# Performance work log

Hardware: AMD Instinct MI355X
Metric: run time of the kernel (lower is better)

## Reference

```python
import math
import jax, jax.numpy as jnp
import numpy as np

B, H, W = 2, 128, 128
HW = H * W
D, NH, NL, KS = 256, 8, 1, 5
NP = KS * KS
HD = D // NH
DFF = 1024
KEEP = 0.25
H_SIZE = 188.0
EPS = 1e-5


def _layernorm(x, g, b):
    m = x.mean(-1, keepdims=True)
    v = ((x - m) ** 2).mean(-1, keepdims=True)
    return (x - m) * jax.lax.rsqrt(v + EPS) * g + b


def _mha(q_in, k_in, v_in, w_qkv, b_qkv, w_o, b_o):
    wq, wk, wv = jnp.split(w_qkv, 3, axis=0)
    bq, bk, bv = jnp.split(b_qkv, 3, axis=0)
    def heads(x, w, b):
        y = x @ w.T + b
        return y.reshape(y.shape[0], y.shape[1], NH, HD)
    q, k, v = heads(q_in, wq, bq), heads(k_in, wk, bk), heads(v_in, wv, bv)
    scores = jnp.einsum('bqhd,bkhd->bhqk', q, k) / math.sqrt(HD)
    attn = jax.nn.softmax(scores, axis=-1)
    out = jnp.einsum('bhqk,bkhd->bqhd', attn, v).reshape(q_in.shape[0], q_in.shape[1], D)
    return out @ w_o.T + b_o


def _bilinear(v, grid):
    # v: (B, HW, NH, HD); grid: (B, LQ, NH, NP, 2) normalized (x, y) in [0,1]
    x = grid[..., 0] * W - 0.5
    y = grid[..., 1] * H - 0.5
    x0 = jnp.floor(x); y0 = jnp.floor(y)
    lx = x - x0; ly = y - y0
    x0i = x0.astype(jnp.int32); y0i = y0.astype(jnp.int32)
    bidx = jnp.arange(v.shape[0])[:, None, None, None]
    hidx = jnp.arange(NH)[None, None, :, None]
    def corner(xi, yi, wgt):
        valid = (xi >= 0) & (xi < W) & (yi >= 0) & (yi < H)  # zero-pad outside
        idx = jnp.clip(yi, 0, H - 1) * W + jnp.clip(xi, 0, W - 1)
        s = v[bidx, idx, hidx]  # (B, LQ, NH, NP, HD)
        return s * (wgt * valid)[..., None]
    return (corner(x0i, y0i, (1 - lx) * (1 - ly))
            + corner(x0i + 1, y0i, lx * (1 - ly))
            + corner(x0i, y0i + 1, (1 - lx) * ly)
            + corner(x0i + 1, y0i + 1, lx * ly))


def _where_to_attend(query, ref_windows, lbw, lbb, sow, sob, kernel_indices):
    Bq, L = ref_windows.shape[:2]
    ob = (query @ lbw.T + lbb).reshape(Bq, L, NH, NL, 4)  # with_rotation=False -> 4 vars
    rw = ref_windows[:, :, None, None, :]  # (B, L, 1, 1, 7)
    ref_boxes = rw[..., jnp.array([0, 1, 3, 4])]
    ref_angles = rw[..., 6:7]
    angles = jnp.broadcast_to(ref_angles, (Bq, L, NH, NL, 1))
    boxes = ref_boxes + ob / 8.0 * ref_boxes[..., jnp.array([2, 3, 2, 3])]
    center = boxes[..., None, :2]  # (B, L, NH, NL, 1, 2)
    size = boxes[..., None, 2:]
    cos_a, sin_a = jnp.cos(angles), jnp.sin(angles)
    rot = jnp.stack([cos_a, -sin_a, sin_a, cos_a], -1).reshape(Bq, L, NH, NL, 1, 2, 2)
    dgrid = (query @ sow.T + sob).reshape(Bq, L, NH, NL, NP, 2) / H_SIZE
    fg = kernel_indices * jax.nn.relu(size)              # (B, L, NH, NL, NP, 2)
    fg = center + (fg[..., None, :] * rot).sum(-1)       # rotate then shift
    return fg + dgrid


def _box_attn(query, value, ref_windows, vpw, vpb, law, lab, lbw, lbb, sow, sob, ow, ob_, kernel_indices):
    Bq, LQ = query.shape[:2]
    LV = value.shape[1]
    v = (value @ vpw.T + vpb).reshape(Bq, LV, NH, HD)
    aw = jax.nn.softmax((query @ law.T + lab).reshape(Bq, LQ, NH, NL * NP), axis=-1)
    aw = aw.reshape(Bq, LQ, NH, NL, NP)
    grid = _where_to_attend(query, ref_windows, lbw, lbb, sow, sob, kernel_indices)
    sampled = _bilinear(v, grid[:, :, :, 0])             # single level (NL=1)
    out = (aw[:, :, :, 0, :, None] * sampled).sum(-2).reshape(Bq, LQ, D)
    return out @ ow.T + ob_


def _forward(src, pos, ref_windows, score_mask, in_proj_w, in_proj_b, mha_out_w, mha_out_b,
             value_proj_w, value_proj_b, linear_attn_w, linear_attn_b, linear_box_w, linear_box_b,
             samp_off_w, samp_off_b, ca_out_w, ca_out_b, lin1_w, lin1_b, lin2_w, lin2_b,
             qn_g, qn_b, n1_g, n1_b, n2_g, n2_b, kernel_indices):
    Bq = src.shape[0]
    fg_num = math.ceil(src.shape[1] * KEEP)
    sel_score, indices = jax.lax.top_k(score_mask, fg_num)
    gather = lambda x, i: jnp.take_along_axis(x, i[..., None], axis=1)
    sel_src = gather(src, indices)
    sel_pos = gather(pos, indices)
    sel_ref = gather(ref_windows, indices)
    q_num = math.ceil(fg_num * KEEP)
    q_idx = jax.lax.top_k(sel_score, q_num)[1]
    q_src = gather(sel_src, q_idx)
    q_pos = gather(sel_pos, q_idx)
    qk = q_src + q_pos
    q2 = _mha(qk, qk, q_src, in_proj_w, in_proj_b, mha_out_w, mha_out_b)
    q_src = _layernorm(q_src + q2, qn_g, qn_b)
    brow = jnp.arange(Bq)[:, None]
    sel_src = sel_src.at[brow, q_idx].set(q_src)
    src2 = _box_attn(sel_src + sel_pos, src, sel_ref, value_proj_w, value_proj_b,
                     linear_attn_w, linear_attn_b, linear_box_w, linear_box_b,
                     samp_off_w, samp_off_b, ca_out_w, ca_out_b, kernel_indices)
    sel_src = _layernorm(sel_src + src2, n1_g, n1_b)
    ff = jax.nn.relu(sel_src @ lin1_w.T + lin1_b) @ lin2_w.T + lin2_b
    sel_src = _layernorm(sel_src + ff, n2_g, n2_b)
    return src.at[brow, indices].set(sel_src)


def setup_inputs() -> dict:
    key = jax.random.key(0)
    ks = jax.random.split(key, 16)
    def w(k, shape):
        return jax.random.normal(k, shape, dtype=jnp.float32) * 0.02
    # deformable sampling-offsets bias init (per-head directional grid)
    thetas = np.arange(NH) * (2.0 * np.pi / NH)
    g = np.stack([np.cos(thetas), np.sin(thetas)], -1)
    g = g / np.abs(g).max(-1, keepdims=True)
    g = np.tile(g.reshape(NH, 1, 1, 2), (1, NL, NP, 1)) * (np.arange(NP) + 1).reshape(1, 1, NP, 1)
    samp_off_b = jnp.asarray(g.reshape(-1), dtype=jnp.float32)
    # fixed kernel indices buffer (odd kernel, (x,y) order, /kernel_size)
    ind = np.linspace(-(KS - 1) / 2, (KS - 1) / 2, KS)
    ii, jj = np.meshgrid(ind, ind, indexing='ij')
    kernel_indices = jnp.asarray(np.stack([jj, ii], -1).reshape(-1, 2) / KS, dtype=jnp.float32)
    return dict(
        src=jax.random.normal(ks[0], (B, HW, D), dtype=jnp.float32),
        pos=jax.random.normal(ks[1], (B, HW, D), dtype=jnp.float32),
        src_shape=jnp.array([[H, W]], dtype=jnp.int32),
        src_start_idx=jnp.zeros((1,), dtype=jnp.int32),
        ref_windows=jax.random.uniform(ks[2], (B, HW, 7), dtype=jnp.float32),
        score_mask=jax.random.normal(ks[3], (B, HW), dtype=jnp.float32),
        in_proj_w=w(ks[4], (3 * D, D)), in_proj_b=jnp.zeros((3 * D,), jnp.float32),
        mha_out_w=w(ks[5], (D, D)), mha_out_b=jnp.zeros((D,), jnp.float32),
        value_proj_w=w(ks[6], (D, D)), value_proj_b=jnp.zeros((D,), jnp.float32),
        linear_attn_w=w(ks[7], (NH * NL * NP, D)), linear_attn_b=jnp.zeros((NH * NL * NP,), jnp.float32),
        linear_box_w=w(ks[8], (NL * NH * 4, D)), linear_box_b=jnp.zeros((NL * NH * 4,), jnp.float32),
        samp_off_w=w(ks[9], (NH * NL * NP * 2, D)), samp_off_b=samp_off_b,
        ca_out_w=w(ks[10], (D, D)), ca_out_b=jnp.zeros((D,), jnp.float32),
        lin1_w=w(ks[11], (DFF, D)), lin1_b=jnp.zeros((DFF,), jnp.float32),
        lin2_w=w(ks[12], (D, DFF)), lin2_b=jnp.zeros((D,), jnp.float32),
        qn_g=jnp.ones((D,), jnp.float32), qn_b=jnp.zeros((D,), jnp.float32),
        n1_g=jnp.ones((D,), jnp.float32), n1_b=jnp.zeros((D,), jnp.float32),
        n2_g=jnp.ones((D,), jnp.float32), n2_b=jnp.zeros((D,), jnp.float32),
        kernel_indices=kernel_indices,
    )


def reference(src, pos, src_shape, src_start_idx, ref_windows, score_mask,
              in_proj_w, in_proj_b, mha_out_w, mha_out_b, value_proj_w, value_proj_b,
              linear_attn_w, linear_attn_b, linear_box_w, linear_box_b, samp_off_w, samp_off_b,
              ca_out_w, ca_out_b, lin1_w, lin1_b, lin2_w, lin2_b,
              qn_g, qn_b, n1_g, n1_b, n2_g, n2_b, kernel_indices):
    # src_shape/src_start_idx are static single-level metadata (H, W closed over)
    return _forward(src, pos, ref_windows, score_mask, in_proj_w, in_proj_b, mha_out_w, mha_out_b,
                    value_proj_w, value_proj_b, linear_attn_w, linear_attn_b, linear_box_w, linear_box_b,
                    samp_off_w, samp_off_b, ca_out_w, ca_out_b, lin1_w, lin1_b, lin2_w, lin2_b,
                    qn_g, qn_b, n1_g, n1_b, n2_g, n2_b, kernel_indices)
```

## Files before the change

### kernel.cpp

```cpp
#include <hip/hip_runtime.h>
#include <hip/hip_bf16.h>
#include <math.h>

#define HW_N   16384
#define DIM    256
#define NSEL   4096
#define NQ     1024
#define NHEAD  8
#define HD     32
#define NP_    25
#define DFF_   1024

#define OFF_SELREF  8448LL
#define OFF_SELSRC  65792LL
#define OFF_SELPOS  2162944LL
#define OFF_QUERY   4260096LL
#define OFF_BIG     6357248LL
#define OFF_WBF     10551552LL
#define OFF_F       14745856LL

__device__ __forceinline__ unsigned int f2s(float f) {
    unsigned int u = __float_as_uint(f);
    return (u & 0x80000000u) ? ~u : (u | 0x80000000u);
}

typedef __bf16 bf16x8 __attribute__((ext_vector_type(8)));
typedef __bf16 bf16x4 __attribute__((ext_vector_type(4)));
typedef float  f32x4  __attribute__((ext_vector_type(4)));

extern "C" __global__ __launch_bounds__(256)
void wcvt_kernel(const float* __restrict__ s0, const float* __restrict__ s1,
                 const float* __restrict__ s2, const float* __restrict__ s3,
                 const float* __restrict__ s4, const float* __restrict__ s5,
                 const float* __restrict__ s6, const float* __restrict__ s7,
                 const float* __restrict__ s8, __hip_bfloat16* __restrict__ dst) {
    const long long g = (long long)blockIdx.x * 256 + threadIdx.x;
    const float* s; long long base;
    if      (g < 196608)  { s = s0; base = 0; }
    else if (g < 262144)  { s = s1; base = 196608; }
    else if (g < 327680)  { s = s2; base = 262144; }
    else if (g < 378880)  { s = s3; base = 327680; }
    else if (g < 387072)  { s = s4; base = 378880; }
    else if (g < 489472)  { s = s5; base = 387072; }
    else if (g < 555008)  { s = s6; base = 489472; }
    else if (g < 817152)  { s = s7; base = 555008; }
    else                  { s = s8; base = 817152; }
    dst[g] = __float2bfloat16(s[g - base]);
}

extern "C" __global__ __launch_bounds__(512)
void topk_hist_kernel(const float* __restrict__ score, unsigned int* __restrict__ hist) {
    const int t = threadIdx.x, bx = blockIdx.x, bb = blockIdx.y;
    const int i = bx * 512 + t;
    unsigned int u = f2s(score[(long long)bb * HW_N + i]);
    atomicAdd(&hist[bb * 8192 + (u >> 19)], 1u);
}

extern "C" __global__ __launch_bounds__(1024)
void topk_scan_kernel(const unsigned int* __restrict__ hist, unsigned int* __restrict__ ctrl) {
    __shared__ unsigned int scan[1024];
    const int t = threadIdx.x, bb = blockIdx.x;
    unsigned int loc[8]; unsigned int lsum = 0u;
    #pragma unroll
    for (int k = 0; k < 8; ++k) { loc[k] = hist[bb * 8192 + t * 8 + k]; lsum += loc[k]; }
    scan[t] = lsum;
    __syncthreads();
    for (int off = 1; off < 1024; off <<= 1) {
        unsigned int v = (t + off < 1024) ? scan[t + off] : 0u;
        __syncthreads();
        scan[t] += v;
        __syncthreads();
    }
    unsigned int nxt = (t < 1023) ? scan[t + 1] : 0u;
    unsigned int run = nxt;
    for (int k = 7; k >= 0; --k) {
        run += loc[k];
        unsigned int above = run - loc[k];
        if (run >= 1024u && above < 1024u) { ctrl[bb * 16 + 0] = (unsigned)(t * 8 + k); ctrl[bb * 16 + 1] = 1024u - above; }
        if (run >= 4096u && above < 4096u) { ctrl[bb * 16 + 2] = (unsigned)(t * 8 + k); ctrl[bb * 16 + 3] = 4096u - above; }
    }
}

extern "C" __global__ __launch_bounds__(1024)
void topk_collect_kernel(const float* __restrict__ score, unsigned int* __restrict__ ctrl,
                         unsigned long long* __restrict__ list1,
                         unsigned long long* __restrict__ list2) {
    const int t = threadIdx.x, bx = blockIdx.x, bb = blockIdx.y;
    const int i = bx * 1024 + t;
    const unsigned int T1 = ctrl[bb * 16 + 0], T2 = ctrl[bb * 16 + 2];
    unsigned int u = f2s(score[(long long)bb * HW_N + i]);
    unsigned int bin = u >> 19;
    unsigned long long key = ((unsigned long long)u << 32) | (unsigned int)(~(unsigned int)i);
    if (bin == T1) {
        unsigned int p = atomicAdd(&ctrl[bb * 16 + 4], 1u);
        if (p < 2048u) list1[bb * 2048 + p] = key;
    }
    if (bin == T2 && T2 != T1) {
        unsigned int p = atomicAdd(&ctrl[bb * 16 + 5], 1u);
        if (p < 2048u) list2[bb * 2048 + p] = key;
    }
}

extern "C" __global__ __launch_bounds__(1024)
void topk_classify_kernel(const float* __restrict__ score, unsigned int* __restrict__ ctrl,
                          const unsigned long long* __restrict__ list1,
                          const unsigned long long* __restrict__ list2,
                          int* __restrict__ idx_out) {
    __shared__ unsigned int cA, cB, baseA, baseB;
    const int t = threadIdx.x, bx = blockIdx.x, bb = blockIdx.y;
    const int i = bx * 1024 + t;
    if (t == 0) { cA = 0u; cB = 0u; }
    __syncthreads();
    const unsigned int T1 = ctrl[bb * 16 + 0], need1 = ctrl[bb * 16 + 1];
    const unsigned int T2 = ctrl[bb * 16 + 2], need2 = ctrl[bb * 16 + 3];
    const unsigned int c1 = min(ctrl[bb * 16 + 4], 2048u);
    const unsigned int c2 = min(ctrl[bb * 16 + 5], 2048u);
    unsigned int u = f2s(score[(long long)bb * HW_N + i]);
    unsigned int bin = u >> 19;
    unsigned long long key = ((unsigned long long)u << 32) | (unsigned int)(~(unsigned int)i);
    bool inA = false, inB = false;
    if (bin > T1) {
        inA = true;
    } else if (bin == T1) {
        unsigned int r = 0;
        for (unsigned int q = 0; q < c1; ++q) r += (list1[bb * 2048 + q] > key) ? 1u : 0u;
        if (r < need1) inA = true;
        else if (T2 == T1) inB = (r < need2);
        else inB = true;
    } else if (bin > T2) {
        inB = true;
    } else if (bin == T2) {
        unsigned int r = 0;
        for (unsigned int q = 0; q < c2; ++q) r += (list2[bb * 2048 + q] > key) ? 1u : 0u;
        inB = (r < need2);
    }
    unsigned int sA = 0u, sB = 0u;
    if (inA) sA = atomicAdd(&cA, 1u);
    if (inB) sB = atomicAdd(&cB, 1u);
    __syncthreads();
    if (t == 0) {
        baseA = atomicAdd(&ctrl[bb * 16 + 6], cA);
        baseB = atomicAdd(&ctrl[bb * 16 + 7], cB);
    }
    __syncthreads();
    if (inA) idx_out[bb * NSEL + baseA + sA] = i;
    if (inB) idx_out[bb * NSEL + 1024 + baseB + sB] = i;
}

extern "C" __global__ __launch_bounds__(256)
void gather_kernel(const float* __restrict__ src, const float* __restrict__ pos,
                   const float* __restrict__ refw, const int* __restrict__ idx,
                   float* __restrict__ selsrc, float* __restrict__ selpos,
                   float* __restrict__ selref, float* __restrict__ qk) {
    const int s = blockIdx.x, bb = blockIdx.y, t = threadIdx.x;
    const int i = idx[bb * NSEL + s];
    const long long so = ((long long)(bb * NSEL + s)) * DIM;
    const long long go = ((long long)(bb * HW_N + i)) * DIM;
    float sv = src[go + t], pv = pos[go + t];
    selsrc[so + t] = sv;
    selpos[so + t] = pv;
    if (s < NQ) qk[((long long)(bb * NQ + s)) * DIM + t] = sv + pv;
    if (t < 7)
        selref[(long long)(bb * NSEL + s) * 7 + t] = refw[(long long)(bb * HW_N + i) * 7 + t];
}

extern "C" __global__ __launch_bounds__(256)
void gemm_kernel(const void* __restrict__ Avp, long long sA,
                 const __hip_bfloat16* __restrict__ W, const float* __restrict__ bias,
                 float* __restrict__ C, long long sC,
                 int M, int N, int K, int relu, int omode, int amode) {
    __shared__ __hip_bfloat16 As[64][72];
    __shared__ __hip_bfloat16 Ws[64][72];
    const int t = threadIdx.x;
    const int n0 = blockIdx.x * 64, m0 = blockIdx.y * 64;
    const long long zoff = (long long)blockIdx.z * sC;
    const int lane = t & 63, wv = t >> 6;
    const int mw = (wv >> 1) * 32, nw = (wv & 1) * 32;
    const int fr = lane & 15;
    const int fk = (lane >> 4) * 8;
    const int sr = t >> 2;
    const int sk = (t & 3) * 16;

    f32x4 acc[2][2];
    #pragma unroll
    for (int i = 0; i < 2; ++i)
        #pragma unroll
        for (int j = 0; j < 2; ++j) acc[i][j] = {0.f, 0.f, 0.f, 0.f};

    const bool wok = (n0 + sr) < N;
    for (int k0 = 0; k0 < K; k0 += 64) {
        uint4 wa = make_uint4(0u, 0u, 0u, 0u), wb = make_uint4(0u, 0u, 0u, 0u);
        if (wok) {
            const __hip_bfloat16* wp = W + (long long)(n0 + sr) * K + k0 + sk;
            wa = *(const uint4*)wp;
            wb = *(const uint4*)(wp + 8);
        }
        if (amode) {
            const __hip_bfloat16* ap = (const __hip_bfloat16*)Avp
                + (long long)blockIdx.z * sA + (long long)(m0 + sr) * K + k0 + sk;
            uint4 aa = *(const uint4*)ap;
            uint4 ab = *(const uint4*)(ap + 8);
            __syncthreads();
            *(uint4*)&As[sr][sk] = aa;
            *(uint4*)&As[sr][sk + 8] = ab;
            *(uint4*)&Ws[sr][sk] = wa;
            *(uint4*)&Ws[sr][sk + 8] = wb;
        } else {
            const float* ap = (const float*)Avp
                + (long long)blockIdx.z * sA + (long long)(m0 + sr) * K + k0 + sk;
            float av[16];
            #pragma unroll
            for (int q = 0; q < 4; ++q) {
                float4 v = *(const float4*)(ap + q * 4);
                av[q * 4 + 0] = v.x; av[q * 4 + 1] = v.y; av[q * 4 + 2] = v.z; av[q * 4 + 3] = v.w;
            }
            __syncthreads();
            #pragma unroll
            for (int q = 0; q < 16; ++q) As[sr][sk + q] = __float2bfloat16(av[q]);
            *(uint4*)&Ws[sr][sk] = wa;
            *(uint4*)&Ws[sr][sk + 8] = wb;
        }
        __syncthreads();
        #pragma unroll
        for (int kk = 0; kk < 64; kk += 32) {
            bf16x8 a0 = *(const bf16x8*)&As[mw + fr][kk + fk];
            bf16x8 a1 = *(const bf16x8*)&As[mw + 16 + fr][kk + fk];
            bf16x8 b0 = *(const bf16x8*)&Ws[nw + fr][kk + fk];
            bf16x8 b1 = *(const bf16x8*)&Ws[nw + 16 + fr][kk + fk];
            acc[0][0] = __builtin_amdgcn_mfma_f32_16x16x32_bf16(a0, b0, acc[0][0], 0, 0, 0);
            acc[0][1] = __builtin_amdgcn_mfma_f32_16x16x32_bf16(a0, b1, acc[0][1], 0, 0, 0);
            acc[1][0] = __builtin_amdgcn_mfma_f32_16x16x32_bf16(a1, b0, acc[1][0], 0, 0, 0);
            acc[1][1] = __builtin_amdgcn_mfma_f32_16x16x32_bf16(a1, b1, acc[1][1], 0, 0, 0);
        }
    }
    const int crow = (lane >> 4) * 4;
    #pragma unroll
    for (int mi = 0; mi < 2; ++mi) {
        #pragma unroll
        for (int ni = 0; ni < 2; ++ni) {
            const int col = n0 + nw + ni * 16 + fr;
            if (col < N) {
                const float bv = bias ? bias[col] : 0.f;
                #pragma unroll
                for (int r = 0; r < 4; ++r) {
                    const int row = m0 + mw + mi * 16 + crow + r;
                    float v = acc[mi][ni][r] + bv;
                    if (relu) v = fmaxf(v, 0.f);
                    if (omode == 0) {
                        C[zoff + (long long)row * N + col] = v;
                    } else if (omode == 1) {
                        ((__hip_bfloat16*)C)[zoff + (long long)row * N + col] = __float2bfloat16(v);
                    } else if (omode == 2) {
                        ((__hip_bfloat16*)C)[zoff + (long long)col * M + row] = __float2bfloat16(v);
                    } else {
                        ((__hip_bfloat16*)C)[zoff + ((long long)(col >> 5) * 16384 + row) * 32 + (col & 31)]
                            = __float2bfloat16(v);
                    }
                }
            }
        }
    }
}

extern "C" __global__ __launch_bounds__(256)
void attn_kernel(const __hip_bfloat16* __restrict__ qkb,
                 const __hip_bfloat16* __restrict__ vT,
                 float* __restrict__ attout) {
    __shared__ __hip_bfloat16 pb[16][1048];
    __shared__ float redm[4][16];
    __shared__ float reds[4][16];
    __shared__ float redo[4][16][33];
    const int t = threadIdx.x;
    const int qt = blockIdx.x, h = blockIdx.y, bb = blockIdx.z;
    const int q0 = qt * 16;
    const int lane = t & 63, wv = t >> 6;
    const int fr = lane & 15, g = lane >> 4;
    const int kbase = wv * 256;
    const float scale = 0.17677669529663687f;

    bf16x8 qfrag = *(const bf16x8*)(qkb + ((long long)(bb * NQ + q0 + fr)) * 512 + h * HD + g * 8);

    f32x4 sfr[16];
    #pragma unroll
    for (int kt = 0; kt < 16; ++kt) {
        const int key0 = kbase + kt * 16;
        bf16x8 kf = *(const bf16x8*)(qkb + ((long long)(bb * NQ + key0 + fr)) * 512 + 256 + h * HD + g * 8);
        f32x4 z = {0.f, 0.f, 0.f, 0.f};
        sfr[kt] = __builtin_amdgcn_mfma_f32_16x16x32_bf16(qfrag, kf, z, 0, 0, 0);
    }
    #pragma unroll
    for (int kt = 0; kt < 16; ++kt)
        #pragma unroll
        for (int r = 0; r < 4; ++r) sfr[kt][r] *= scale;

    #pragma unroll
    for (int r = 0; r < 4; ++r) {
        float mx = -1e30f;
        #pragma unroll
        for (int kt = 0; kt < 16; ++kt) mx = fmaxf(mx, sfr[kt][r]);
        #pragma unroll
        for (int mm = 1; mm <= 8; mm <<= 1) mx = fmaxf(mx, __shfl_xor(mx, mm, 64));
        float sm = 0.f;
        #pragma unroll
        for (int kt = 0; kt < 16; ++kt) sm += expf(sfr[kt][r] - mx);
        #pragma unroll
        for (int mm = 1; mm <= 8; mm <<= 1) sm += __shfl_xor(sm, mm, 64);
        if (fr == 0) { redm[wv][4 * g + r] = mx; reds[wv][4 * g + r] = sm; }
    }
    __syncthreads();

    float gm[4], gl[4];
    #pragma unroll
    for (int r = 0; r < 4; ++r) {
        const int q = 4 * g + r;
        float mm = fmaxf(fmaxf(redm[0][q], redm[1][q]), fmaxf(redm[2][q], redm[3][q]));
        float ll = 0.f;
        #pragma unroll
        for (int w2 = 0; w2 < 4; ++w2) ll += reds[w2][q] * expf(redm[w2][q] - mm);
        gm[r] = mm; gl[r] = 1.f / ll;
    }
    #pragma unroll
    for (int kt = 0; kt < 16; ++kt) {
        #pragma unroll
        for (int r = 0; r < 4; ++r) {
            float p = expf(sfr[kt][r] - gm[r]) * gl[r];
            pb[4 * g + r][kbase + kt * 16 + fr] = __float2bfloat16(p);
        }
    }

    f32x4 o0 = {0.f, 0.f, 0.f, 0.f}, o1 = {0.f, 0.f, 0.f, 0.f};
    const __hip_bfloat16* vbase = vT + ((long long)bb * DIM + h * HD) * 1024;
    #pragma unroll
    for (int ks = 0; ks < 8; ++ks) {
        const int key0 = kbase + ks * 32 + g * 8;
        bf16x8 pf = *(const bf16x8*)&pb[fr][key0];
        bf16x8 v0 = *(const bf16x8*)(vbase + (long long)fr * 1024 + key0);
        bf16x8 v1 = *(const bf16x8*)(vbase + (long long)(16 + fr) * 1024 + key0);
        o0 = __builtin_amdgcn_mfma_f32_16x16x32_bf16(pf, v0, o0, 0, 0, 0);
        o1 = __builtin_amdgcn_mfma_f32_16x16x32_bf16(pf, v1, o1, 0, 0, 0);
    }

    #pragma unroll
    for (int r = 0; r < 4; ++r) {
        redo[wv][4 * g + r][fr] = o0[r];
        redo[wv][4 * g + r][16 + fr] = o1[r];
    }
    __syncthreads();
    #pragma unroll
    for (int i = 0; i < 2; ++i) {
        const int idx = t + i * 256;
        const int q = idx >> 5, d = idx & 31;
        float v = redo[0][q][d] + redo[1][q][d] + redo[2][q][d] + redo[3][q][d];
        attout[((long long)(bb * NQ + q0 + q)) * DIM + h * HD + d] = v;
    }
}

extern "C" __global__ __launch_bounds__(256)
void ln_kernel(const float* __restrict__ X, long long sx,
               const float* __restrict__ R, long long sr,
               const float* __restrict__ g, const float* __restrict__ bta,
               float* __restrict__ O, long long so) {
    __shared__ float red[4];
    const int row = blockIdx.x, bb = blockIdx.y, t = threadIdx.x;
    float x = X[(long long)bb * sx + (long long)row * DIM + t]
            + R[(long long)bb * sr + (long long)row * DIM + t];
    float v = x;
    #pragma unroll
    for (int m = 32; m >= 1; m >>= 1) v += __shfl_xor(v, m, 64);
    if ((t & 63) == 0) red[t >> 6] = v;
    __syncthreads();
    float mean = (red[0] + red[1] + red[2] + red[3]) * (1.f / 256.f);
    __syncthreads();
    float d = x - mean;
    v = d * d;
    #pragma unroll
    for (int m = 32; m >= 1; m >>= 1) v += __shfl_xor(v, m, 64);
    if ((t & 63) == 0) red[t >> 6] = v;
    __syncthreads();
    float var = (red[0] + red[1] + red[2] + red[3]) * (1.f / 256.f);
    O[(long long)bb * so + (long long)row * DIM + t] = d * rsqrtf(var + 1e-5f) * g[t] + bta[t];
}

extern "C" __global__ __launch_bounds__(256)
void addq_kernel(const float* __restrict__ a, const float* __restrict__ b2, float* __restrict__ o) {
    long long i = (long long)blockIdx.x * 256 + threadIdx.x;
    o[i] = a[i] + b2[i];
}

extern "C" __global__ __launch_bounds__(256)
void boxattn_kernel(const float* __restrict__ aw, const float* __restrict__ ob,
                    const float* __restrict__ dgrid, const float* __restrict__ selref,
                    const __hip_bfloat16* __restrict__ vp, const float* __restrict__ kidx,
                    float* __restrict__ boxout) {
    __shared__ float aw_s[200];
    __shared__ float ob_s[32];
    __shared__ float ref_s[7];
    __shared__ float ki_s[50];
    __shared__ float box_s[8][6];
    __shared__ float mx_s[8];
    __shared__ float inv_s[8];
    __shared__ float wq_s[200];
    __shared__ int   i4_s[800];
    __shared__ float w4_s[800];
    __shared__ float red4[4][8][32];
    const int t = threadIdx.x;
    const int s = blockIdx.x, bb = blockIdx.y;
    const long long base = (long long)(bb * NSEL + s);
    if (t < 200) aw_s[t] = aw[base * 200 + t];
    if (t < 32)  ob_s[t] = ob[base * 32 + t];
    if (t < 7)   ref_s[t] = selref[base * 7 + t];
    if (t < 50)  ki_s[t] = kidx[t];
    __syncthreads();

    if (t < 8) {
        float mx = -1e30f;
        #pragma unroll
        for (int p = 0; p < NP_; ++p) mx = fmaxf(mx, aw_s[t * NP_ + p]);
        mx_s[t] = mx;
        const float r0 = ref_s[0], r1 = ref_s[1], r3 = ref_s[3], r4 = ref_s[4], r6 = ref_s[6];
        box_s[t][0] = r0 + ob_s[t * 4 + 0] * 0.125f * r3;
        box_s[t][1] = r1 + ob_s[t * 4 + 1] * 0.125f * r4;
        box_s[t][2] = fmaxf(r3 + ob_s[t * 4 + 2] * 0.125f * r3, 0.f);
        box_s[t][3] = fmaxf(r4 + ob_s[t * 4 + 3] * 0.125f * r4, 0.f);
        box_s[t][4] = cosf(r6);
        box_s[t][5] = sinf(r6);
    }
    __syncthreads();

    if (t < 200) {
        const int h = t / NP_, p = t - h * NP_;
        const float w = expf(aw_s[t] - mx_s[h]);
        wq_s[t] = w;
        const float cx = box_s[h][0], cy = box_s[h][1];
        const float sw = box_s[h][2], sh = box_s[h][3];
        const float ca = box_s[h][4], sa = box_s[h][5];
        const float fx = ki_s[p * 2 + 0] * sw;
        const float fy = ki_s[p * 2 + 1] * sh;
        const float gx = cx + ca * fx - sa * fy + dgrid[base * 400 + 2 * t + 0] * (1.f / 188.f);
        const float gy = cy + sa * fx + ca * fy + dgrid[base * 400 + 2 * t + 1] * (1.f / 188.f);
        const float x = gx * 128.f - 0.5f;
        const float y = gy * 128.f - 0.5f;
        const float x0f = floorf(x), y0f = floorf(y);
        const float lx = x - x0f, ly = y - y0f;
        const int x0 = (int)x0f, y0 = (int)y0f;
        #pragma unroll
        for (int c = 0; c < 4; ++c) {
            const int xi = x0 + (c & 1);
            const int yi = y0 + (c >> 1);
            const float wgt = ((c & 1) ? lx : 1.f - lx) * ((c >> 1) ? ly : 1.f - ly);
            const bool valid = (xi >= 0) & (xi < 128) & (yi >= 0) & (yi < 128);
            const int cxi = min(max(xi, 0), 127);
            const int cyi = min(max(yi, 0), 127);
            i4_s[t * 4 + c] = cyi * 128 + cxi;
            w4_s[t * 4 + c] = w * (valid ? wgt : 0.f);
        }
    }
    __syncthreads();
    if (t < 8) {
        float sm = 0.f;
        #pragma unroll
        for (int p = 0; p < NP_; ++p) sm += wq_s[t * NP_ + p];
        inv_s[t] = 1.f / sm;
    }
    __syncthreads();

    {
        const int lane = t & 63, wv = t >> 6;
        const int h2 = lane >> 3, q = lane & 7;
        const __hip_bfloat16* vb = vp + ((long long)(bb * 8 + h2) * 16384) * 32 + q * 4;
        float a0 = 0.f, a1 = 0.f, a2 = 0.f, a3 = 0.f;
        for (int j = wv; j < 100; j += 4) {
            const int e = h2 * 100 + j;
            const int pix = i4_s[e];
            const float w = w4_s[e];
            bf16x4 v = *(const bf16x4*)(vb + (long long)pix * 32);
            a0 += w * (float)v[0];
            a1 += w * (float)v[1];
            a2 += w * (float)v[2];
            a3 += w * (float)v[3];
        }
        red4[wv][h2][q * 4 + 0] = a0;
        red4[wv][h2][q * 4 + 1] = a1;
        red4[wv][h2][q * 4 + 2] = a2;
        red4[wv][h2][q * 4 + 3] = a3;
    }
    __syncthreads();
    {
        const int h = t >> 5, d = t & 31;
        float v = red4[0][h][d] + red4[1][h][d] + red4[2][h][d] + red4[3][h][d];
        boxout[base * DIM + h * HD + d] = v * inv_s[h];
    }
}

extern "C" __global__ __launch_bounds__(256)
void scatter_kernel(const int* __restrict__ idx, const float* __restrict__ sel,
                    float* __restrict__ out) {
    const int s = blockIdx.x, bb = blockIdx.y, t = threadIdx.x;
    const int i = idx[bb * NSEL + s];
    out[((long long)(bb * HW_N + i)) * DIM + t] = sel[((long long)(bb * NSEL + s)) * DIM + t];
}

extern "C" void kernel_launch(void* const* d_in, const int* in_sizes, int n_in,
                              void* d_out, int out_size, void* d_ws, size_t ws_size,
                              hipStream_t stream) {
    const float* src          = (const float*)d_in[0];
    const float* pos          = (const float*)d_in[1];
    const float* refw         = (const float*)d_in[4];
    const float* score        = (const float*)d_in[5];
    const float* in_proj_w    = (const float*)d_in[6];
    const float* in_proj_b    = (const float*)d_in[7];
    const float* mha_out_w    = (const float*)d_in[8];
    const float* mha_out_b    = (const float*)d_in[9];
    const float* value_proj_w = (const float*)d_in[10];
    const float* value_proj_b = (const float*)d_in[11];
    const float* lin_attn_w   = (const float*)d_in[12];
    const float* lin_attn_b   = (const float*)d_in[13];
    const float* lin_box_w    = (const float*)d_in[14];
    const float* lin_box_b    = (const float*)d_in[15];
    const float* samp_off_w   = (const float*)d_in[16];
    const float* samp_off_b   = (const float*)d_in[17];
    const float* ca_out_w     = (const float*)d_in[18];
    const float* ca_out_b     = (const float*)d_in[19];
    const float* lin1_w       = (const float*)d_in[20];
    const float* lin1_b       = (const float*)d_in[21];
    const float* lin2_w       = (const float*)d_in[22];
    const float* lin2_b       = (const float*)d_in[23];
    const float* qn_g         = (const float*)d_in[24];
    const float* qn_b         = (const float*)d_in[25];
    const float* n1_g         = (const float*)d_in[26];
    const float* n1_b         = (const float*)d_in[27];
    const float* n2_g         = (const float*)d_in[28];
    const float* n2_b         = (const float*)d_in[29];
    const float* kidx         = (const float*)d_in[30];

    float* w = (float*)d_ws;
    int* idxp = (int*)d_ws;
    float* selref = w + OFF_SELREF;
    float* selsrc = w + OFF_SELSRC;
    float* selpos = w + OFF_SELPOS;
    float* boxout = w + OFF_SELPOS;
    float* query  = w + OFF_QUERY;
    float* src2   = w + OFF_QUERY;
    __hip_bfloat16* vproj  = (__hip_bfloat16*)(w + OFF_BIG);
    __hip_bfloat16* ffntb  = (__hip_bfloat16*)(w + OFF_BIG);
    __hip_bfloat16* wbf    = (__hip_bfloat16*)(w + OFF_WBF);
    float* qk     = w + OFF_F;
    __hip_bfloat16* qkb = (__hip_bfloat16*)(w + OFF_F + 524288);
    __hip_bfloat16* vT  = (__hip_bfloat16*)(w + OFF_F + 1572864);
    float* attout = w + OFF_F + 2097152;
    float* q2     = w + OFF_F + 2621440;
    float* aw     = w + OFF_F;
    float* obuf   = w + OFF_F + 1638400;
    float* dgrid  = w + OFF_F + 1900544;
    float* ff     = w + OFF_F;
    unsigned int* hist2 = (unsigned int*)(w + OFF_F);
    unsigned int* ctrl2 = hist2 + 16384;
    unsigned long long* list1 = (unsigned long long*)(hist2 + 16448);
    unsigned long long* list2 = list1 + 2 * 2048;
    float* out    = (float*)d_out;

    const long long W_INPROJ = 0, W_MHAOUT = 196608, W_VALUE = 262144,
                    W_LATTN = 327680, W_LBOX = 378880, W_SOFF = 387072,
                    W_CAOUT = 489472, W_LIN1 = 555008, W_LIN2 = 817152;

    hipMemcpyAsync(d_out, src, (size_t)2 * HW_N * DIM * sizeof(float),
                   hipMemcpyDeviceToDevice, stream);

    wcvt_kernel<<<4216, 256, 0, stream>>>(in_proj_w, mha_out_w, value_proj_w,
                                          lin_attn_w, lin_box_w, samp_off_w,
                                          ca_out_w, lin1_w, lin2_w, wbf);

    hipMemsetAsync(hist2, 0, 16448 * sizeof(unsigned int), stream);
    topk_hist_kernel<<<dim3(32, 2), 512, 0, stream>>>(score, hist2);
    topk_scan_kernel<<<2, 1024, 0, stream>>>(hist2, ctrl2);
    topk_collect_kernel<<<dim3(16, 2), 1024, 0, stream>>>(score, ctrl2, list1, list2);
    topk_classify_kernel<<<dim3(16, 2), 1024, 0, stream>>>(score, ctrl2, list1, list2, idxp);

    gather_kernel<<<dim3(NSEL, 2), 256, 0, stream>>>(src, pos, refw, idxp,
                                                     selsrc, selpos, selref, qk);
    gemm_kernel<<<dim3(8, 16, 2), 256, 0, stream>>>(qk, 262144LL, wbf + W_INPROJ, in_proj_b,
                                                    (float*)qkb, 524288LL, NQ, 512, 256, 0, 1, 0);
    gemm_kernel<<<dim3(4, 16, 2), 256, 0, stream>>>(selsrc, 1048576LL, wbf + W_INPROJ + 512 * 256,
                                                    in_proj_b + 512, (float*)vT, 262144LL, NQ, 256, 256, 0, 2, 0);
    attn_kernel<<<dim3(64, 8, 2), 256, 0, stream>>>(qkb, vT, attout);
    gemm_kernel<<<dim3(4, 16, 2), 256, 0, stream>>>(attout, 262144LL, wbf + W_MHAOUT, mha_out_b,
                                                    q2, 262144LL, NQ, 256, 256, 0, 0, 0);
    ln_kernel<<<dim3(NQ, 2), 256, 0, stream>>>(selsrc, 1048576LL, q2, 262144LL,
                                               qn_g, qn_b, selsrc, 1048576LL);
    addq_kernel<<<8192, 256, 0, stream>>>(selsrc, selpos, query);
    gemm_kernel<<<dim3(4, 256, 2), 256, 0, stream>>>(src, 4194304LL, wbf + W_VALUE, value_proj_b,
                                                     (float*)vproj, 4194304LL, HW_N, 256, 256, 0, 3, 0);
    gemm_kernel<<<dim3(4, 64, 2), 256, 0, stream>>>(query, 1048576LL, wbf + W_LATTN, lin_attn_b,
                                                    aw, 819200LL, NSEL, 200, 256, 0, 0, 0);
    gemm_kernel<<<dim3(1, 64, 2), 256, 0, stream>>>(query, 1048576LL, wbf + W_LBOX, lin_box_b,
                                                    obuf, 131072LL, NSEL, 32, 256, 0, 0, 0);
    gemm_kernel<<<dim3(7, 64, 2), 256, 0, stream>>>(query, 1048576LL, wbf + W_SOFF, samp_off_b,
                                                    dgrid, 1638400LL, NSEL, 400, 256, 0, 0, 0);
    boxattn_kernel<<<dim3(NSEL, 2), 256, 0, stream>>>(aw, obuf, dgrid, selref, vproj, kidx, boxout);
    gemm_kernel<<<dim3(4, 64, 2), 256, 0, stream>>>(boxout, 1048576LL, wbf + W_CAOUT, ca_out_b,
                                                    src2, 1048576LL, NSEL, 256, 256, 0, 0, 0);
    ln_kernel<<<dim3(NSEL, 2), 256, 0, stream>>>(selsrc, 1048576LL, src2, 1048576LL,
                                                 n1_g, n1_b, selsrc, 1048576LL);
    gemm_kernel<<<dim3(16, 64, 2), 256, 0, stream>>>(selsrc, 1048576LL, wbf + W_LIN1, lin1_b,
                                                     (float*)ffntb, 4194304LL, NSEL, DFF_, 256, 1, 1, 0);
    gemm_kernel<<<dim3(4, 64, 2), 256, 0, stream>>>(ffntb, 4194304LL, wbf + W_LIN2, lin2_b,
                                                    ff, 1048576LL, NSEL, 256, DFF_, 0, 0, 1);
    ln_kernel<<<dim3(NSEL, 2), 256, 0, stream>>>(selsrc, 1048576LL, ff, 1048576LL,
                                                 n2_g, n2_b, selsrc, 1048576LL);
    scatter_kernel<<<dim3(NSEL, 2), 256, 0, stream>>>(idxp, selsrc, out);
}
```

Baseline: 460.5 us.

## Restructure box-attention gather with 512 threads, 16-byte loads and shuffle reduction

The bilinear gather in boxattn_kernel now runs with 512 threads per block. Each thread issues up to 7 independent 8-element bf16 loads, all kept in flight before accumulation, and the partial sums are reduced with warp shuffles. This replaces the LDS partial-sum array, an extra barrier and the separate normalisation pass. It targets memory latency in the random-access gather, at the cost of more registers, more threads per block, and some wasted padded loads.

```diff
diff --git a/kernel.cpp b/kernel.cpp
--- a/kernel.cpp
+++ b/kernel.cpp
@@ -387,7 +387,7 @@
     o[i] = a[i] + b2[i];
 }
 
-extern "C" __global__ __launch_bounds__(256)
+extern "C" __global__ __launch_bounds__(512)
 void boxattn_kernel(const float* __restrict__ aw, const float* __restrict__ ob,
                     const float* __restrict__ dgrid, const float* __restrict__ selref,
                     const __hip_bfloat16* __restrict__ vp, const float* __restrict__ kidx,
@@ -398,11 +398,9 @@
     __shared__ float ki_s[50];
     __shared__ float box_s[8][6];
     __shared__ float mx_s[8];
-    __shared__ float inv_s[8];
     __shared__ float wq_s[200];
     __shared__ int   i4_s[800];
     __shared__ float w4_s[800];
-    __shared__ float red4[4][8][32];
     const int t = threadIdx.x;
     const int s = blockIdx.x, bb = blockIdx.y;
     const long long base = (long long)(bb * NSEL + s);
@@ -456,39 +454,40 @@
         }
     }
     __syncthreads();
-    if (t < 8) {
-        float sm = 0.f;
-        #pragma unroll
-        for (int p = 0; p < NP_; ++p) sm += wq_s[t * NP_ + p];
-        inv_s[t] = 1.f / sm;
-    }
-    __syncthreads();
 
     {
-        const int lane = t & 63, wv = t >> 6;
-        const int h2 = lane >> 3, q = lane & 7;
-        const __hip_bfloat16* vb = vp + ((long long)(bb * 8 + h2) * 16384) * 32 + q * 4;
-        float a0 = 0.f, a1 = 0.f, a2 = 0.f, a3 = 0.f;
-        for (int j = wv; j < 100; j += 4) {
-            const int e = h2 * 100 + j;
-            const int pix = i4_s[e];
-            const float w = w4_s[e];
-            bf16x4 v = *(const bf16x4*)(vb + (long long)pix * 32);
-            a0 += w * (float)v[0];
-            a1 += w * (float)v[1];
-            a2 += w * (float)v[2];
-            a3 += w * (float)v[3];
-        }
-        red4[wv][h2][q * 4 + 0] = a0;
-        red4[wv][h2][q * 4 + 1] = a1;
-        red4[wv][h2][q * 4 + 2] = a2;
-        red4[wv][h2][q * 4 + 3] = a3;
-    }
-    __syncthreads();
-    {
-        const int h = t >> 5, d = t & 31;
-        float v = red4[0][h][d] + red4[1][h][d] + red4[2][h][d] + red4[3][h][d];
-        boxout[base * DIM + h * HD + d] = v * inv_s[h];
+        const int h2 = t >> 6;
+        const int oct = (t >> 4) & 3;
+        const int stream = t & 15;
+        const __hip_bfloat16* vb = vp + ((long long)(bb * 8 + h2) * 16384) * 32 + oct * 8;
+        bf16x8 vv[7];
+        float  wls[7];
+        #pragma unroll
+        for (int u = 0; u < 7; ++u) {
+            const int j = stream + u * 16;
+            const bool ok = (j < 100);
+            const int e = h2 * 100 + (ok ? j : 0);
+            vv[u]  = *(const bf16x8*)(vb + (long long)i4_s[e] * 32);
+            wls[u] = ok ? w4_s[e] : 0.f;
+        }
+        float a[8] = {0.f, 0.f, 0.f, 0.f, 0.f, 0.f, 0.f, 0.f};
+        #pragma unroll
+        for (int u = 0; u < 7; ++u)
+            #pragma unroll
+            for (int k = 0; k < 8; ++k) a[k] += wls[u] * (float)vv[u][k];
+        #pragma unroll
+        for (int m = 1; m <= 8; m <<= 1)
+            #pragma unroll
+            for (int k = 0; k < 8; ++k) a[k] += __shfl_xor(a[k], m, 64);
+        if (stream == 0) {
+            float inv = 0.f;
+            #pragma unroll
+            for (int p = 0; p < NP_; ++p) inv += wq_s[h2 * NP_ + p];
+            inv = 1.f / inv;
+            #pragma unroll
+            for (int k = 0; k < 8; ++k)
+                boxout[base * DIM + h2 * HD + oct * 8 + k] = a[k] * inv;
+        }
     }
 }
 
@@ -596,7 +595,7 @@
                                                     obuf, 131072LL, NSEL, 32, 256, 0, 0, 0);
     gemm_kernel<<<dim3(7, 64, 2), 256, 0, stream>>>(query, 1048576LL, wbf + W_SOFF, samp_off_b,
                                                     dgrid, 1638400LL, NSEL, 400, 256, 0, 0, 0);
-    boxattn_kernel<<<dim3(NSEL, 2), 256, 0, stream>>>(aw, obuf, dgrid, selref, vproj, kidx, boxout);
+    boxattn_kernel<<<dim3(NSEL, 2), 512, 0, stream>>>(aw, obuf, dgrid, selref, vproj, kidx, boxout);
     gemm_kernel<<<dim3(4, 64, 2), 256, 0, stream>>>(boxout, 1048576LL, wbf + W_CAOUT, ca_out_b,
                                                     src2, 1048576LL, NSEL, 256, 256, 0, 0, 0);
     ln_kernel<<<dim3(NSEL, 2), 256, 0, stream>>>(selsrc, 1048576LL, src2, 1048576LL,
```

Result: slower. 470.7 us (+2.2%).
